# Optimization experiments

Hardware: AMD Instinct MI355X
Metric: run time of the kernel (lower is better)

The kernel has to match this reference:

```python
import jax, jax.numpy as jnp
import numpy as np

B, LINS, LHIS, LACT = 128, 64, 128, 32
VOCAB, ACTSZ = 2000, 100
INS_H, INS_E = 256, 128
ACT_E, ACT_IN, ACT_H = 128, 512, 512
POS_E, COL_E, COL_H = 32, 32, 32
ENV = 7 * (POS_E + COL_H)  # 448


def _lstm_cell(h, c, x, Wih, Whh, bih, bhh):
    # torch LSTM gate order: i, f, g, o
    g = x @ Wih.T + h @ Whh.T + bih + bhh
    i, f, gg, o = jnp.split(g, 4, axis=-1)
    c = jax.nn.sigmoid(f) * c + jax.nn.sigmoid(i) * jnp.tanh(gg)
    h = jax.nn.sigmoid(o) * jnp.tanh(c)
    return h, c


def _run_lstm(xs, Wih, Whh, bih, bhh):
    # xs: [T, N, D] -> hs: [T, N, H], zero initial state (torch default)
    N = xs.shape[1]
    H = Whh.shape[1]
    h0 = jnp.zeros((N, H), xs.dtype)

    def step(carry, x):
        h, c = carry
        h, c = _lstm_cell(h, c, x, Wih, Whh, bih, bhh)
        return (h, c), h

    _, hs = jax.lax.scan(step, (h0, h0), xs)
    return hs


def _bilstm_encode(tokens, emb, Wf, Uf, bf1, bf2, Wb, Ub, bb1, bb2):
    xs = emb[tokens].transpose(1, 0, 2)            # [L, B, E]
    hf = _run_lstm(xs, Wf, Uf, bf1, bf2)           # [L, B, H]
    hb = _run_lstm(xs[::-1], Wb, Ub, bb1, bb2)[::-1]
    return jnp.concatenate([hf, hb], -1).transpose(1, 0, 2)  # [B, L, 2H]


def _env_encode(tokens, color_emb, pos_emb, Wih, Whh, bih, bhh):
    # tokens: [B, 35] = 7 beakers x (id + 4 color slots)
    t = tokens.reshape(B, 7, 5)
    col = color_emb[t[:, :, 1:5]]                  # [B, 7, 4, COL_E]
    xs = col.reshape(B * 7, 4, COL_E).transpose(1, 0, 2)  # [4, B*7, COL_E]
    h_last = _run_lstm(xs, Wih, Whh, bih, bhh)[-1].reshape(B, 7, COL_H)
    pos = jnp.broadcast_to(pos_emb[None], (B, 7, POS_E))
    return jnp.concatenate([pos, h_last], -1).reshape(B, 7 * (POS_E + COL_H))


def _attend(A, H, q):
    # Faithful to attend(): scores = sum_k (H @ W)[b,l,k] * q[b,k]; softmax over l;
    # A = H @ W is query-independent so it is hoisted out of the decode loop.
    a = jax.nn.softmax(jnp.einsum('blk,bk->bl', A, q), axis=1)
    return jnp.einsum('bl,bld->bd', a, H)


def _forward(ins_tokens, his_tokens, actions, cur_env, ini_env,
             enc_emb, enc_Wih_f, enc_Whh_f, enc_bih_f, enc_bhh_f,
             enc_Wih_b, enc_Whh_b, enc_bih_b, enc_bhh_b,
             color_emb, pos_emb, ws_Wih, ws_Whh, ws_bih, ws_bhh,
             act_emb, W_c, W_p, W_sb1, W_sb2, W_sc1, W_sc2,
             Wbd_W, Wbd_b, dec_Wih, dec_Whh, dec_bih, dec_bhh,
             h2a_W, h2a_b, h0, c0):
    ins_enc = _bilstm_encode(ins_tokens, enc_emb, enc_Wih_f, enc_Whh_f, enc_bih_f,
                             enc_bhh_f, enc_Wih_b, enc_Whh_b, enc_bih_b, enc_bhh_b)
    his_enc = _bilstm_encode(his_tokens, enc_emb, enc_Wih_f, enc_Whh_f, enc_bih_f,
                             enc_bhh_f, enc_Wih_b, enc_Whh_b, enc_bih_b, enc_bhh_b)
    cur_ctx = _env_encode(cur_env, color_emb, pos_emb, ws_Wih, ws_Whh, ws_bih, ws_bhh)
    ini_ctx = _env_encode(ini_env, color_emb, pos_emb, ws_Wih, ws_Whh, ws_bih, ws_bhh)

    X = act_emb[actions]                            # [B, T, ACT_E]
    # Query-independent projections, hoisted out of the per-step loop (same math).
    A_c = jnp.einsum('bld,dk->blk', ins_enc, W_c)   # [B, LINS, ACT_H]
    A_p = jnp.einsum('bld,dk->blk', his_enc, W_p)   # [B, LHIS, ACT_H+2*INS_H]
    K = ACT_H + 2 * INS_H
    ini_rep = jnp.broadcast_to(ini_ctx[:, None, :], (B, LACT, ENV))
    cur_rep = jnp.broadcast_to(cur_ctx[:, None, :], (B, LACT, ENV))
    A_b1 = jnp.broadcast_to((ini_ctx @ W_sb1)[:, None, :], (B, LACT, K))
    A_b2 = jnp.broadcast_to((ini_ctx @ W_sb2)[:, None, :], (B, LACT, K))
    A_c1 = jnp.broadcast_to((cur_ctx @ W_sc1)[:, None, :], (B, LACT, K))
    A_c2 = jnp.broadcast_to((cur_ctx @ W_sc2)[:, None, :], (B, LACT, K))

    def step(carry, x_t):
        h, c = carry
        z_c = _attend(A_c, ins_enc, h)              # [B, 2*INS_H]
        q = jnp.concatenate([h, z_c], -1)           # [B, ACT_H+2*INS_H]
        z_p = _attend(A_p, his_enc, q)
        z_s1 = jnp.concatenate([_attend(A_b1, ini_rep, q),
                                _attend(A_b2, ini_rep, q)], -1)
        z_sk = jnp.concatenate([_attend(A_c1, cur_rep, q),
                                _attend(A_c2, cur_rep, q)], -1)
        hk1 = jnp.concatenate([z_c, z_p, z_s1, z_sk, x_t], -1)  # [B, 2944]
        hk = jnp.tanh(hk1 @ Wbd_W.T + Wbd_b)        # [B, ACT_IN]
        h, c = _lstm_cell(h, c, hk, dec_Wih, dec_Whh, dec_bih, dec_bhh)
        return (h, c), h

    _, outs = jax.lax.scan(step, (h0, c0), X.transpose(1, 0, 2))
    logits = outs.transpose(1, 0, 2) @ h2a_W.T + h2a_b  # [B, LACT, ACTSZ]
    return logits


def setup_inputs() -> dict:
    root = jax.random.key(0)
    ki = iter(jax.random.split(root, 40))

    def nrm(shape, s=0.05):
        return jax.random.normal(next(ki), shape, dtype=jnp.float32) * s

    inp = {}
    inp['ins_tokens'] = jax.random.randint(next(ki), (B, LINS), 0, VOCAB)
    inp['his_tokens'] = jax.random.randint(next(ki), (B, LHIS), 0, VOCAB)
    inp['actions'] = jax.random.randint(next(ki), (B, LACT), 0, ACTSZ)
    inp['cur_env'] = jax.random.randint(next(ki), (B, 35), 0, 7)
    inp['ini_env'] = jax.random.randint(next(ki), (B, 35), 0, 7)
    inp['enc_emb'] = nrm((VOCAB, INS_E))
    inp['enc_Wih_f'] = nrm((4 * INS_H, INS_E))
    inp['enc_Whh_f'] = nrm((4 * INS_H, INS_H))
    inp['enc_bih_f'] = nrm((4 * INS_H,))
    inp['enc_bhh_f'] = nrm((4 * INS_H,))
    inp['enc_Wih_b'] = nrm((4 * INS_H, INS_E))
    inp['enc_Whh_b'] = nrm((4 * INS_H, INS_H))
    inp['enc_bih_b'] = nrm((4 * INS_H,))
    inp['enc_bhh_b'] = nrm((4 * INS_H,))
    inp['color_emb'] = nrm((7, COL_E))
    inp['pos_emb'] = nrm((7, POS_E))
    inp['ws_Wih'] = nrm((4 * COL_H, COL_E))
    inp['ws_Whh'] = nrm((4 * COL_H, COL_H))
    inp['ws_bih'] = nrm((4 * COL_H,))
    inp['ws_bhh'] = nrm((4 * COL_H,))
    inp['act_emb'] = nrm((ACTSZ, ACT_E))
    inp['W_c'] = nrm((2 * INS_H, ACT_H))
    inp['W_p'] = nrm((2 * INS_H, 2 * INS_H + ACT_H))
    inp['W_sb1'] = nrm((ENV, ACT_H + 2 * INS_H))
    inp['W_sb2'] = nrm((ENV, ACT_H + 2 * INS_H))
    inp['W_sc1'] = nrm((ENV, ACT_H + 2 * INS_H))
    inp['W_sc2'] = nrm((ENV, ACT_H + 2 * INS_H))
    inp['Wbd_W'] = nrm((ACT_IN, 4 * ENV + 4 * INS_H + ACT_E))
    inp['Wbd_b'] = nrm((ACT_IN,))
    inp['dec_Wih'] = nrm((4 * ACT_H, ACT_IN))
    inp['dec_Whh'] = nrm((4 * ACT_H, ACT_H))
    inp['dec_bih'] = nrm((4 * ACT_H,))
    inp['dec_bhh'] = nrm((4 * ACT_H,))
    inp['h2a_W'] = nrm((ACTSZ, ACT_H))
    inp['h2a_b'] = nrm((ACTSZ,))
    inp['h0'] = nrm((B, ACT_H))
    inp['c0'] = nrm((B, ACT_H))
    return inp


def reference(ins_tokens, his_tokens, actions, cur_env, ini_env,
              enc_emb, enc_Wih_f, enc_Whh_f, enc_bih_f, enc_bhh_f,
              enc_Wih_b, enc_Whh_b, enc_bih_b, enc_bhh_b,
              color_emb, pos_emb, ws_Wih, ws_Whh, ws_bih, ws_bhh,
              act_emb, W_c, W_p, W_sb1, W_sb2, W_sc1, W_sc2,
              Wbd_W, Wbd_b, dec_Wih, dec_Whh, dec_bih, dec_bhh,
              h2a_W, h2a_b, h0, c0):
    return _forward(ins_tokens, his_tokens, actions, cur_env, ini_env,
                    enc_emb, enc_Wih_f, enc_Whh_f, enc_bih_f, enc_bhh_f,
                    enc_Wih_b, enc_Whh_b, enc_bih_b, enc_bhh_b,
                    color_emb, pos_emb, ws_Wih, ws_Whh, ws_bih, ws_bhh,
                    act_emb, W_c, W_p, W_sb1, W_sb2, W_sc1, W_sc2,
                    Wbd_W, Wbd_b, dec_Wih, dec_Whh, dec_bih, dec_bhh,
                    h2a_W, h2a_b, h0, c0)
```

## Files before the change

kernel.cpp:

```cpp
#include <hip/hip_runtime.h>


typedef unsigned short u16;
typedef __attribute__((ext_vector_type(8))) short bf16x8;
typedef __attribute__((ext_vector_type(4))) float f32x4;

#define DEVFN static __device__ __forceinline__

DEVFN float bf2f(u16 u) {
  unsigned int x = ((unsigned int)u) << 16;
  float f; __builtin_memcpy(&f, &x, 4); return f;
}
DEVFN u16 f2bf(float f) {
  unsigned int x; __builtin_memcpy(&x, &f, 4);
  x = (x + 0x7fffu + ((x >> 16) & 1u)) >> 16;
  return (u16)x;
}
DEVFN float sigf(float x) { return 1.f / (1.f + __expf(-x)); }
DEVFN bf16x8 load8(const u16* p) { return *(const bf16x8*)p; }
DEVFN int clampi(int v, int lo, int hi) { return v < lo ? lo : (v > hi ? hi : v); }

struct GemmArgs {
  const u16* A; int lda; int M;
  const u16* W; int ldw; int N; int K;
  void* out; int ldc;
  const float* bias;
  const float* hk_base; const float* proj_act; const int* actions; int t;
};

template <int EPI>
__global__ __launch_bounds__(256) void gemm_k(GemmArgs g) {
  int lane = threadIdx.x & 63;
  int wave = threadIdx.x >> 6;
  int col = lane & 15, q = lane >> 4;
  int m0 = blockIdx.x * 64 + (wave >> 1) * 32;
  int n0 = blockIdx.y * 64 + (wave & 1) * 32;
  f32x4 acc[2][2] = {};
  int rA[2] = { m0 + col, m0 + 16 + col };
  int rB[2] = { n0 + col, n0 + 16 + col };
  bool gA[2] = { rA[0] < g.M, rA[1] < g.M };
  bool gB[2] = { rB[0] < g.N, rB[1] < g.N };
  const u16* pA[2]; const u16* pB[2];
#pragma unroll
  for (int i = 0; i < 2; i++) {
    pA[i] = g.A + (size_t)(gA[i] ? rA[i] : 0) * g.lda + q * 8;
    pB[i] = g.W + (size_t)(gB[i] ? rB[i] : 0) * g.ldw + q * 8;
  }
  bf16x8 zf = {0,0,0,0,0,0,0,0};
  for (int k = 0; k < g.K; k += 32) {
    bf16x8 a0 = gA[0] ? load8(pA[0] + k) : zf;
    bf16x8 a1 = gA[1] ? load8(pA[1] + k) : zf;
    bf16x8 b0 = gB[0] ? load8(pB[0] + k) : zf;
    bf16x8 b1 = gB[1] ? load8(pB[1] + k) : zf;
    acc[0][0] = __builtin_amdgcn_mfma_f32_16x16x32_bf16(a0, b0, acc[0][0], 0, 0, 0);
    acc[0][1] = __builtin_amdgcn_mfma_f32_16x16x32_bf16(a0, b1, acc[0][1], 0, 0, 0);
    acc[1][0] = __builtin_amdgcn_mfma_f32_16x16x32_bf16(a1, b0, acc[1][0], 0, 0, 0);
    acc[1][1] = __builtin_amdgcn_mfma_f32_16x16x32_bf16(a1, b1, acc[1][1], 0, 0, 0);
  }
#pragma unroll
  for (int mi = 0; mi < 2; mi++)
#pragma unroll
    for (int ni = 0; ni < 2; ni++)
#pragma unroll
      for (int r = 0; r < 4; r++) {
        int m = m0 + mi * 16 + q * 4 + r;
        int n = n0 + ni * 16 + col;
        if (m >= g.M || n >= g.N) continue;
        float v = acc[mi][ni][r];
        if constexpr (EPI == 0) {
          if (g.bias) v += g.bias[n];
          ((float*)g.out)[(size_t)m * g.ldc + n] = v;
        } else {
          ((u16*)g.out)[(size_t)m * g.ldc + n] = f2bf(v);
        }
      }
}

template <int EPI>
__global__ __launch_bounds__(256) void gemm32_k(GemmArgs g) {
  int lane = threadIdx.x & 63;
  int wave = threadIdx.x >> 6;
  int col = lane & 15, q = lane >> 4;
  int m0 = blockIdx.x * 32 + (wave >> 1) * 16;
  int n0 = blockIdx.y * 32 + (wave & 1) * 16;
  f32x4 acc = {};
  int rA = m0 + col, rB = n0 + col;
  bool gA = rA < g.M, gB = rB < g.N;
  const u16* pA = g.A + (size_t)(gA ? rA : 0) * g.lda + q * 8;
  const u16* pB = g.W + (size_t)(gB ? rB : 0) * g.ldw + q * 8;
  bf16x8 zf = {0,0,0,0,0,0,0,0};
  for (int k = 0; k < g.K; k += 32) {
    bf16x8 a = gA ? load8(pA + k) : zf;
    bf16x8 b = gB ? load8(pB + k) : zf;
    acc = __builtin_amdgcn_mfma_f32_16x16x32_bf16(a, b, acc, 0, 0, 0);
  }
#pragma unroll
  for (int r = 0; r < 4; r++) {
    int m = m0 + q * 4 + r;
    int n = n0 + col;
    if (m >= g.M || n >= g.N) continue;
    float v = acc[r];
    if constexpr (EPI == 0) {
      if (g.bias) v += g.bias[n];
      ((float*)g.out)[(size_t)m * g.ldc + n] = v;
    } else {
      int act = clampi(g.actions[m * 32 + g.t], 0, 99);
      v += g.hk_base[m * 512 + n] + g.proj_act[(size_t)act * 512 + n];
      ((u16*)g.out)[(size_t)m * g.ldc + n] = f2bf(tanhf(v));
    }
  }
}

__global__ __launch_bounds__(256) void up_split(
    const u16* qbuf, const u16* wp, float* u_p2) {
  int lane = threadIdx.x & 63;
  int wave = threadIdx.x >> 6;
  int col = lane & 15, q = lane >> 4;
  int half = blockIdx.y >> 4;
  int by = blockIdx.y & 15;
  int m0 = blockIdx.x * 32 + (wave >> 1) * 16;
  int n0 = by * 32 + (wave & 1) * 16;
  f32x4 acc = {};
  const u16* pA = qbuf + (size_t)(m0 + col) * 1024 + half * 512 + q * 8;
  const u16* pB = wp + (size_t)(n0 + col) * 1024 + half * 512 + q * 8;
  for (int k = 0; k < 512; k += 32) {
    acc = __builtin_amdgcn_mfma_f32_16x16x32_bf16(load8(pA + k), load8(pB + k), acc, 0, 0, 0);
  }
  float* out = u_p2 + (size_t)half * 128 * 512;
#pragma unroll
  for (int r = 0; r < 4; r++) {
    int m = m0 + q * 4 + r;
    int n = n0 + col;
    out[(size_t)m * 512 + n] = acc[r];
  }
}

__global__ __launch_bounds__(256) void dec_gates_cell32(
    const u16* zin_cur, const u16* Wih, const u16* Whh, const float* bias_int,
    float* c_ws, u16* zin_nxt, u16* qbuf, u16* outs, int t) {
  int lane = threadIdx.x & 63, wave = threadIdx.x >> 6;
  int col = lane & 15, q = lane >> 4;
  int m0 = blockIdx.x * 32 + (wave >> 1) * 16;
  int n0 = blockIdx.y * 32 + (wave & 1) * 16;
  f32x4 acc = {};
  const u16* pA = zin_cur + (size_t)(m0 + col) * 1024 + q * 8;
  int r = n0 + col;
  int src = (r & 3) * 512 + (r >> 2);
  const u16* pI = Wih + (size_t)src * 512 + q * 8;
  const u16* pH = Whh + (size_t)src * 512 + q * 8;
  for (int k = 0; k < 512; k += 32) {
    acc = __builtin_amdgcn_mfma_f32_16x16x32_bf16(load8(pA + k), load8(pI + k), acc, 0, 0, 0);
  }
  for (int k = 0; k < 512; k += 32) {
    acc = __builtin_amdgcn_mfma_f32_16x16x32_bf16(load8(pA + 512 + k), load8(pH + k), acc, 0, 0, 0);
  }
  __shared__ float ls[32][36];
#pragma unroll
  for (int rr = 0; rr < 4; rr++) {
    int ml = (wave >> 1) * 16 + q * 4 + rr;
    int nl = (wave & 1) * 16 + col;
    ls[ml][nl] = acc[rr] + bias_int[blockIdx.y * 32 + nl];
  }
  __syncthreads();
  int m = threadIdx.x & 31, jloc = threadIdx.x >> 5;
  int gm = blockIdx.x * 32 + m;
  int j = blockIdx.y * 8 + jloc;
  float gi = ls[m][jloc * 4 + 0];
  float gf = ls[m][jloc * 4 + 1];
  float gg = ls[m][jloc * 4 + 2];
  float go = ls[m][jloc * 4 + 3];
  float cn = sigf(gf) * c_ws[gm * 512 + j] + sigf(gi) * tanhf(gg);
  c_ws[gm * 512 + j] = cn;
  float hn = sigf(go) * tanhf(cn);
  u16 hb = f2bf(hn);
  zin_nxt[(size_t)gm * 1024 + 512 + j] = hb;
  qbuf[(size_t)gm * 1024 + j] = hb;
  outs[((size_t)gm * 32 + t) * 512 + j] = hb;
}

struct CvtJob { const float* src; u16* dst; int R; int C; int ld; int c0; int tr; int blk0; };
struct CvtJobs { CvtJob j[15]; int njobs; };

__global__ void cvt_all(CvtJobs a) {
  int bid = blockIdx.x;
  int ji = 0;
  while (ji + 1 < a.njobs && bid >= a.j[ji + 1].blk0) ji++;
  CvtJob jb = a.j[ji];
  int idx = (bid - jb.blk0) * 256 + threadIdx.x;
  int n = jb.R * jb.C;
  if (idx >= n) return;
  int r = idx / jb.C, c = idx - r * jb.C;
  float v = jb.src[(size_t)r * jb.ld + jb.c0 + c];
  if (jb.tr) jb.dst[(size_t)c * jb.R + r] = f2bf(v);
  else jb.dst[idx] = f2bf(v);
}

__global__ void prep_small(
    const float* bih_f, const float* bhh_f, float* bias_f,
    const float* bih_b, const float* bhh_b, float* bias_b,
    const float* Wbd_b, float* bwbd,
    const float* h2a_b, float* bh2a,
    const float* dec_bih, const float* dec_bhh, float* bdecint,
    const float* h0, const float* c0, u16* zin0, u16* qbuf, float* c_ws) {
  int i = blockIdx.x * 256 + threadIdx.x;
  if (i < 1024) bias_f[i] = bih_f[i] + bhh_f[i];
  else if (i < 2048) { int k = i - 1024; bias_b[k] = bih_b[k] + bhh_b[k]; }
  else if (i < 2560) { int k = i - 2048; bwbd[k] = Wbd_b[k]; }
  else if (i < 2660) { int k = i - 2560; bh2a[k] = h2a_b[k]; }
  else if (i < 4708) {
    int r = i - 2660;
    int j = r >> 2, gg = r & 3;
    bdecint[r] = dec_bih[gg * 512 + j] + dec_bhh[gg * 512 + j];
  } else if (i < 4708 + 128 * 512) {
    int k = i - 4708;
    int b = k >> 9, d = k & 511;
    u16 hv = f2bf(h0[k]);
    zin0[(size_t)b * 1024 + 512 + d] = hv;
    qbuf[(size_t)b * 1024 + d] = hv;
    c_ws[k] = c0[k];
  }
}

__global__ void wsum_build(const float* Wbd, u16* Wsum) {
  int idx = blockIdx.x * 256 + threadIdx.x;
  int n = idx / 896, j = idx % 896;
  int c1 = (j < 448) ? (1024 + j) : (1920 + (j - 448));
  int c2 = c1 + 448;
  Wsum[idx] = f2bf(Wbd[(size_t)n * 2944 + c1] + Wbd[(size_t)n * 2944 + c2]);
}

__global__ __launch_bounds__(256) void env_encode(
    const int* cur_env, const int* ini_env,
    const float* color_emb, const float* pos_emb,
    const float* wih, const float* whh, const float* bih, const float* bhh,
    u16* ctx_cat) {
  __shared__ float s_wih[128 * 33], s_whh[128 * 33], s_b[128], s_col[7 * 32];
  __shared__ float h_lds[8][33];
  int tid = threadIdx.x;
  for (int i = tid; i < 128 * 32; i += 256) {
    int r = i >> 5, k2 = i & 31;
    s_wih[r * 33 + k2] = wih[i];
    s_whh[r * 33 + k2] = whh[i];
  }
  for (int i = tid; i < 128; i += 256) s_b[i] = bih[i] + bhh[i];
  for (int i = tid; i < 224; i += 256) s_col[i] = color_emb[i];
  int sl = tid >> 5, j = tid & 31;
  int gseq = blockIdx.x * 8 + sl;
  int e = gseq / 896, rem = gseq % 896;
  int b = rem / 7, p = rem % 7;
  const int* env = e ? ini_env : cur_env;
  int eoff = e ? 0 : 448;
  h_lds[sl][j] = 0.f;
  __syncthreads();
  float cj = 0.f, hj = 0.f;
  for (int st = 0; st < 4; st++) {
    int tok = clampi(env[b * 35 + p * 5 + 1 + st], 0, 6);
    const float* x = &s_col[tok * 32];
    float pi = s_b[j], pf = s_b[32 + j], pg = s_b[64 + j], po = s_b[96 + j];
    for (int k = 0; k < 32; k++) {
      float xk = x[k], hk = h_lds[sl][k];
      pi += s_wih[j * 33 + k] * xk + s_whh[j * 33 + k] * hk;
      pf += s_wih[(32 + j) * 33 + k] * xk + s_whh[(32 + j) * 33 + k] * hk;
      pg += s_wih[(64 + j) * 33 + k] * xk + s_whh[(64 + j) * 33 + k] * hk;
      po += s_wih[(96 + j) * 33 + k] * xk + s_whh[(96 + j) * 33 + k] * hk;
    }
    cj = sigf(pf) * cj + sigf(pi) * tanhf(pg);
    hj = sigf(po) * tanhf(cj);
    __syncthreads();
    h_lds[sl][j] = hj;
    __syncthreads();
  }
  size_t base = (size_t)b * 896 + eoff + p * 64;
  ctx_cat[base + j] = f2bf(pos_emb[p * 32 + j]);
  ctx_cat[base + 32 + j] = f2bf(hj);
}

#define HBUF ((size_t)4 * 128 * 256)
__global__ __launch_bounds__(128) void enc_step3(
    int t, int chainbase,
    const int* ins_tok, const int* his_tok,
    const float* projE_f, const float* projE_b,
    const u16* whh_f, const u16* whh_b,
    const float* bias_f, const float* bias_b,
    u16* h_enc, float* c_enc,
    u16* ins_enc, u16* his_enc) {
  int chain = chainbase + (blockIdx.x >> 6);
  int sub = blockIdx.x & 63;
  int sgrp = sub >> 3, jq = sub & 7;
  int w = threadIdx.x >> 6, lane = threadIdx.x & 63;
  int col = lane & 15, q = lane >> 4;
  int dir = chain & 1, his = chain >> 1;
  int L = his ? 128 : 64;
  const int* toks = his ? his_tok : ins_tok;
  int t_x = dir ? (L - 1 - t) : t;
  const float* projE = dir ? projE_b : projE_f;
  const u16* whh = dir ? whh_b : whh_f;
  const float* bias = dir ? bias_b : bias_f;
  const u16* h_rd = h_enc + ((size_t)((t & 1) ^ 1)) * HBUF + (size_t)chain * 128 * 256;
  u16* h_wr = h_enc + ((size_t)(t & 1)) * HBUF + (size_t)chain * 128 * 256;
  float* c_g = c_enc + (size_t)chain * 128 * 256;
  u16* out = his ? his_enc : ins_enc;

  int jw = jq * 32 + w * 16;
  f32x4 acc[4] = {};
  if (t > 0) {
    const u16* hrow = h_rd + (size_t)(sgrp * 16 + col) * 256 + q * 8;
    const u16* wrow[4];
#pragma unroll
    for (int G = 0; G < 4; G++) wrow[G] = whh + (size_t)(G * 256 + jw + col) * 256 + q * 8;
    for (int k = 0; k < 256; k += 32) {
      bf16x8 a = load8(hrow + k);
#pragma unroll
      for (int G = 0; G < 4; G++) {
        bf16x8 bb = load8(wrow[G] + k);
        acc[G] = __builtin_amdgcn_mfma_f32_16x16x32_bf16(a, bb, acc[G], 0, 0, 0);
      }
    }
  }
  int j = jw + col;
  float bi = bias[j], bf = bias[256 + j], bg = bias[512 + j], bo = bias[768 + j];
#pragma unroll
  for (int r = 0; r < 4; r++) {
    int s = q * 4 + r;
    int b = sgrp * 16 + s;
    int tok = clampi(toks[b * L + t_x], 0, 1999);
    const float* px = projE + (size_t)tok * 1024;
    float pi = acc[0][r] + px[j] + bi;
    float pf = acc[1][r] + px[256 + j] + bf;
    float pg = acc[2][r] + px[512 + j] + bg;
    float po = acc[3][r] + px[768 + j] + bo;
    float cold = (t > 0) ? c_g[b * 256 + j] : 0.f;
    float cn = sigf(pf) * cold + sigf(pi) * tanhf(pg);
    float hn = sigf(po) * tanhf(cn);
    c_g[b * 256 + j] = cn;
    u16 hb = f2bf(hn);
    h_wr[b * 256 + j] = hb;
    out[((size_t)b * L + t_x) * 512 + dir * 256 + j] = hb;
  }
}

__global__ __launch_bounds__(512) void attn1(
    const u16* A_c, const u16* insenc, u16* qattn, u16* qbuf) {
  int b = blockIdx.x, tid = threadIdx.x;
  __shared__ float su[512], red[512], aw[64];
  __shared__ float zacc[8][512];
  su[tid] = bf2f(qbuf[(size_t)b * 1024 + tid]);
  __syncthreads();
  {
    int l = tid >> 3, part = tid & 7;
    const u16* row = A_c + ((size_t)b * 64 + l) * 512 + part * 64;
    float s = 0.f;
    for (int k = 0; k < 64; k += 8) {
      bf16x8 v = load8(row + k);
#pragma unroll
      for (int e = 0; e < 8; e++) s += bf2f((u16)v[e]) * su[part * 64 + k + e];
    }
    red[tid] = s;
  }
  __syncthreads();
  if (tid < 64) {
    float sc = 0.f;
#pragma unroll
    for (int i = 0; i < 8; i++) sc += red[tid * 8 + i];
    float m = sc;
    for (int off = 32; off > 0; off >>= 1) m = fmaxf(m, __shfl_xor(m, off));
    float e = __expf(sc - m);
    float sm = e;
    for (int off = 32; off > 0; off >>= 1) sm += __shfl_xor(sm, off);
    aw[tid] = e / sm;
  }
  __syncthreads();
  {
    int part = tid >> 6, chunk = tid & 63;
    float a[8] = {};
    for (int l = part * 8; l < part * 8 + 8; l++) {
      bf16x8 v = load8(insenc + ((size_t)b * 64 + l) * 512 + chunk * 8);
      float w = aw[l];
#pragma unroll
      for (int e = 0; e < 8; e++) a[e] += w * bf2f((u16)v[e]);
    }
#pragma unroll
    for (int e = 0; e < 8; e++) zacc[part][chunk * 8 + e] = a[e];
  }
  __syncthreads();
  {
    float z = zacc[0][tid] + zacc[1][tid] + zacc[2][tid] + zacc[3][tid]
            + zacc[4][tid] + zacc[5][tid] + zacc[6][tid] + zacc[7][tid];
    u16 zb = f2bf(z);
    qattn[(size_t)b * 1024 + tid] = zb;
    qbuf[(size_t)b * 1024 + 512 + tid] = zb;
  }
}

__global__ __launch_bounds__(512) void attn2(
    const float* u_p2, const u16* hisenc, u16* qattn) {
  int b = blockIdx.x, tid = threadIdx.x;
  __shared__ float su[512], red[512], aw[128], mr[2];
  __shared__ float zacc[8][512];
  su[tid] = u_p2[(size_t)b * 512 + tid] + u_p2[65536 + (size_t)b * 512 + tid];
  __syncthreads();
  {
    int l = tid >> 2, part = tid & 3;
    const u16* row = hisenc + ((size_t)b * 128 + l) * 512 + part * 128;
    float s = 0.f;
    for (int k = 0; k < 128; k += 8) {
      bf16x8 v = load8(row + k);
#pragma unroll
      for (int e = 0; e < 8; e++) s += bf2f((u16)v[e]) * su[part * 128 + k + e];
    }
    red[tid] = s;
  }
  __syncthreads();
  float sc = 0.f;
  if (tid < 128) sc = red[tid * 4] + red[tid * 4 + 1] + red[tid * 4 + 2] + red[tid * 4 + 3];
  __syncthreads();
  if (tid < 128) red[tid] = sc;
  __syncthreads();
  if (tid < 64) {
    float m = fmaxf(red[tid], red[tid + 64]);
    for (int off = 32; off > 0; off >>= 1) m = fmaxf(m, __shfl_xor(m, off));
    if (tid == 0) mr[0] = m;
  }
  __syncthreads();
  float ex = 0.f;
  if (tid < 128) { ex = __expf(sc - mr[0]); red[tid] = ex; }
  __syncthreads();
  if (tid < 64) {
    float s2 = red[tid] + red[tid + 64];
    for (int off = 32; off > 0; off >>= 1) s2 += __shfl_xor(s2, off);
    if (tid == 0) mr[1] = s2;
  }
  __syncthreads();
  if (tid < 128) aw[tid] = ex / mr[1];
  __syncthreads();
  {
    int part = tid >> 6, chunk = tid & 63;
    float a[8] = {};
    for (int l = part * 16; l < part * 16 + 16; l++) {
      bf16x8 v = load8(hisenc + ((size_t)b * 128 + l) * 512 + chunk * 8);
      float w = aw[l];
#pragma unroll
      for (int e = 0; e < 8; e++) a[e] += w * bf2f((u16)v[e]);
    }
#pragma unroll
    for (int e = 0; e < 8; e++) zacc[part][chunk * 8 + e] = a[e];
  }
  __syncthreads();
  {
    float z = zacc[0][tid] + zacc[1][tid] + zacc[2][tid] + zacc[3][tid]
            + zacc[4][tid] + zacc[5][tid] + zacc[6][tid] + zacc[7][tid];
    qattn[(size_t)b * 1024 + 512 + tid] = f2bf(z);
  }
}

extern "C" void kernel_launch(void* const* d_in, const int* in_sizes, int n_in,
                              void* d_out, int out_size, void* d_ws, size_t ws_size,
                              hipStream_t stream) {
  const int* ins_tok = (const int*)d_in[0];
  const int* his_tok = (const int*)d_in[1];
  const int* actions = (const int*)d_in[2];
  const int* cur_env = (const int*)d_in[3];
  const int* ini_env = (const int*)d_in[4];
  const float* enc_emb = (const float*)d_in[5];
  const float* Wih_f = (const float*)d_in[6];
  const float* Whh_f = (const float*)d_in[7];
  const float* bih_f = (const float*)d_in[8];
  const float* bhh_f = (const float*)d_in[9];
  const float* Wih_b = (const float*)d_in[10];
  const float* Whh_b = (const float*)d_in[11];
  const float* bih_b = (const float*)d_in[12];
  const float* bhh_b = (const float*)d_in[13];
  const float* color_emb = (const float*)d_in[14];
  const float* pos_emb = (const float*)d_in[15];
  const float* ws_Wih = (const float*)d_in[16];
  const float* ws_Whh = (const float*)d_in[17];
  const float* ws_bih = (const float*)d_in[18];
  const float* ws_bhh = (const float*)d_in[19];
  const float* act_emb = (const float*)d_in[20];
  const float* W_c = (const float*)d_in[21];
  const float* W_p = (const float*)d_in[22];
  const float* Wbd_W = (const float*)d_in[27];
  const float* Wbd_b = (const float*)d_in[28];
  const float* dec_Wih = (const float*)d_in[29];
  const float* dec_Whh = (const float*)d_in[30];
  const float* dec_bih = (const float*)d_in[31];
  const float* dec_bhh = (const float*)d_in[32];
  const float* h2a_W = (const float*)d_in[33];
  const float* h2a_b = (const float*)d_in[34];
  const float* h0 = (const float*)d_in[35];
  const float* c0 = (const float*)d_in[36];
  (void)in_sizes; (void)n_in; (void)out_size; (void)ws_size;

  char* ws = (char*)d_ws;
  size_t off = 0;
  auto alloc = [&](size_t bytes) -> char* {
    char* p = ws + off;
    off = (off + bytes + 255) & ~(size_t)255;
    return p;
  };
  u16* insenc   = (u16*)alloc(8192ull * 512 * 2);
  u16* hisenc   = (u16*)alloc(16384ull * 512 * 2);
  u16* outs     = (u16*)alloc(4096ull * 512 * 2);
  u16* Wsum     = (u16*)alloc(512ull * 896 * 2);
  u16* h_enc    = (u16*)alloc(2 * HBUF * 2);
  float* c_enc  = (float*)alloc(4ull * 128 * 256 * 4);
  float* projact= (float*)alloc(100ull * 512 * 4);
  float* bias_f = (float*)alloc(1024 * 4);
  float* bias_b = (float*)alloc(1024 * 4);
  float* bdecint= (float*)alloc(2048 * 4);
  float* bwbd   = (float*)alloc(512 * 4);
  float* bh2a   = (float*)alloc(128 * 4);
  u16* ctxcat   = (u16*)alloc(128ull * 896 * 2);
  float* hkbase = (float*)alloc(128ull * 512 * 4);
  float* u_p2   = (float*)alloc(2ull * 128 * 512 * 4);
  u16* qbuf     = (u16*)alloc(128ull * 1024 * 2);
  u16* qattn    = (u16*)alloc(128ull * 1024 * 2);
  u16* zin      = (u16*)alloc(2ull * 128 * 1024 * 2);
  float* c_dec  = (float*)alloc(128ull * 512 * 4);
  float* projE_f = (float*)alloc(2000ull * 1024 * 4);
  float* projE_b = (float*)alloc(2000ull * 1024 * 4);
  u16* A_c      = (u16*)alloc(8192ull * 512 * 2);
  u16* emb_bf   = (u16*)alloc(2000ull * 128 * 2);
  u16* wihf_bf  = (u16*)alloc(1024ull * 128 * 2);
  u16* wihb_bf  = (u16*)alloc(1024ull * 128 * 2);
  u16* whhf_bf  = (u16*)alloc(1024ull * 256 * 2);
  u16* whhb_bf  = (u16*)alloc(1024ull * 256 * 2);
  u16* act_bf   = (u16*)alloc(100ull * 128 * 2);
  u16* wcT_bf   = (u16*)alloc(512ull * 512 * 2);
  u16* wp_bf    = (u16*)alloc(512ull * 1024 * 2);
  u16* wbd01_bf = (u16*)alloc(512ull * 1024 * 2);
  u16* wbdx_bf  = (u16*)alloc(512ull * 128 * 2);
  u16* dwih_bf  = (u16*)alloc(2048ull * 512 * 2);
  u16* dwhh_bf  = (u16*)alloc(2048ull * 512 * 2);
  u16* h2a_bf   = (u16*)alloc(100ull * 512 * 2);

  CvtJobs cj{};
  int nb = 0, jn = 0;
  auto addjob = [&](const float* s, u16* d, int R, int C, int ld, int c0c, int tr) {
    cj.j[jn] = { s, d, R, C, ld, c0c, tr, nb };
    nb += (R * C + 255) / 256;
    jn++;
  };
  addjob(enc_emb, emb_bf, 2000, 128, 128, 0, 0);
  addjob(Wih_f, wihf_bf, 1024, 128, 128, 0, 0);
  addjob(Wih_b, wihb_bf, 1024, 128, 128, 0, 0);
  addjob(Whh_f, whhf_bf, 1024, 256, 256, 0, 0);
  addjob(Whh_b, whhb_bf, 1024, 256, 256, 0, 0);
  addjob(act_emb, act_bf, 100, 128, 128, 0, 0);
  addjob(W_c, wcT_bf, 512, 512, 512, 0, 1);
  addjob(W_p, wp_bf, 512, 1024, 1024, 0, 0);
  addjob(Wbd_W, wbd01_bf, 512, 1024, 2944, 0, 0);
  addjob(Wbd_W, wbdx_bf, 512, 128, 2944, 2816, 0);
  addjob(dec_Wih, dwih_bf, 2048, 512, 512, 0, 0);
  addjob(dec_Whh, dwhh_bf, 2048, 512, 512, 0, 0);
  addjob(h2a_W, h2a_bf, 100, 512, 512, 0, 0);
  cj.njobs = jn;
  cvt_all<<<nb, 256, 0, stream>>>(cj);

  prep_small<<<(4708 + 128 * 512 + 255) / 256, 256, 0, stream>>>(
      bih_f, bhh_f, bias_f, bih_b, bhh_b, bias_b,
      Wbd_b, bwbd, h2a_b, bh2a, dec_bih, dec_bhh, bdecint,
      h0, c0, zin, qbuf, c_dec);
  wsum_build<<<1792, 256, 0, stream>>>(Wbd_W, Wsum);

  {
    GemmArgs ge = {};
    ge.A = emb_bf; ge.lda = 128; ge.M = 2000; ge.W = wihf_bf; ge.ldw = 128;
    ge.N = 1024; ge.K = 128; ge.out = projE_f; ge.ldc = 1024;
    gemm_k<0><<<dim3(32, 16), 256, 0, stream>>>(ge);
    ge.W = wihb_bf; ge.out = projE_b;
    gemm_k<0><<<dim3(32, 16), 256, 0, stream>>>(ge);
  }

  GemmArgs gp = {};
  gp.A = act_bf; gp.lda = 128; gp.M = 100; gp.W = wbdx_bf; gp.ldw = 128;
  gp.N = 512; gp.K = 128; gp.out = projact; gp.ldc = 512; gp.bias = bwbd;
  gemm_k<0><<<dim3(2, 8), 256, 0, stream>>>(gp);

  env_encode<<<224, 256, 0, stream>>>(cur_env, ini_env, color_emb, pos_emb,
                                      ws_Wih, ws_Whh, ws_bih, ws_bhh, ctxcat);
  GemmArgs gb = {};
  gb.A = ctxcat; gb.lda = 896; gb.M = 128; gb.W = Wsum; gb.ldw = 896;
  gb.N = 512; gb.K = 896; gb.out = hkbase; gb.ldc = 512;
  gemm_k<0><<<dim3(2, 8), 256, 0, stream>>>(gb);

  for (int t = 0; t < 128; t++) {
    int cb = (t < 64) ? 0 : 2;
    int nbk = (t < 64) ? 256 : 128;
    enc_step3<<<nbk, 128, 0, stream>>>(t, cb, ins_tok, his_tok,
                                       projE_f, projE_b, whhf_bf, whhb_bf,
                                       bias_f, bias_b, h_enc, c_enc,
                                       insenc, hisenc);
  }

  {
    GemmArgs ga = {};
    ga.A = insenc; ga.lda = 512; ga.M = 8192; ga.W = wcT_bf; ga.ldw = 512;
    ga.N = 512; ga.K = 512; ga.out = A_c; ga.ldc = 512;
    gemm_k<1><<<dim3(128, 8), 256, 0, stream>>>(ga);
  }

  for (int t = 0; t < 32; t++) {
    u16* zin_cur = zin + (size_t)(t & 1) * 128 * 1024;
    u16* zin_nxt = zin + (size_t)((t + 1) & 1) * 128 * 1024;
    attn1<<<128, 512, 0, stream>>>(A_c, insenc, qattn, qbuf);
    up_split<<<dim3(4, 32), 256, 0, stream>>>(qbuf, wp_bf, u_p2);
    attn2<<<128, 512, 0, stream>>>(u_p2, hisenc, qattn);
    GemmArgs gh = {};
    gh.A = qattn; gh.lda = 1024; gh.M = 128; gh.W = wbd01_bf; gh.ldw = 1024;
    gh.N = 512; gh.K = 1024; gh.out = zin_cur; gh.ldc = 1024;
    gh.hk_base = hkbase; gh.proj_act = projact; gh.actions = actions; gh.t = t;
    gemm32_k<2><<<dim3(4, 16), 256, 0, stream>>>(gh);
    dec_gates_cell32<<<dim3(4, 64), 256, 0, stream>>>(
        zin_cur, dwih_bf, dwhh_bf, bdecint, c_dec, zin_nxt, qbuf, outs, t);
  }

  GemmArgs gl = {};
  gl.A = outs; gl.lda = 512; gl.M = 4096; gl.W = h2a_bf; gl.ldw = 512;
  gl.N = 100; gl.K = 512; gl.out = d_out; gl.ldc = 100; gl.bias = bh2a;
  gemm32_k<0><<<dim3(128, 4), 256, 0, stream>>>(gl);
}
```

Measured before the change: 2.531 ms.

## Split K and shrink blocks in encoder, decoder cell, and attention projection kernels

The encoder step kernel now uses single-wave blocks with twice as many blocks. The decoder gate/cell kernel splits the K reduction across two waves per tile and sums the partials through LDS. The attention projection splits K into four quarters instead of two, and attn2 sums four partials. The aim is more parallelism and shorter serial MFMA chains in the latency-bound sequential steps. The cost is extra partial-sum traffic, more LDS, and more blocks launched per step.

Result: no change. 2.561 ms (+1.2%).

```diff
diff --git a/kernel.cpp b/kernel.cpp
--- a/kernel.cpp
+++ b/kernel.cpp
@@ -111,22 +111,22 @@
   }
 }
 
-__global__ __launch_bounds__(256) void up_split(
-    const u16* qbuf, const u16* wp, float* u_p2) {
+__global__ __launch_bounds__(256) void up_split4(
+    const u16* qbuf, const u16* wp, float* u_p4) {
   int lane = threadIdx.x & 63;
   int wave = threadIdx.x >> 6;
   int col = lane & 15, q = lane >> 4;
-  int half = blockIdx.y >> 4;
+  int qtr = blockIdx.y >> 4;
   int by = blockIdx.y & 15;
   int m0 = blockIdx.x * 32 + (wave >> 1) * 16;
   int n0 = by * 32 + (wave & 1) * 16;
   f32x4 acc = {};
-  const u16* pA = qbuf + (size_t)(m0 + col) * 1024 + half * 512 + q * 8;
-  const u16* pB = wp + (size_t)(n0 + col) * 1024 + half * 512 + q * 8;
-  for (int k = 0; k < 512; k += 32) {
+  const u16* pA = qbuf + (size_t)(m0 + col) * 1024 + qtr * 256 + q * 8;
+  const u16* pB = wp + (size_t)(n0 + col) * 1024 + qtr * 256 + q * 8;
+  for (int k = 0; k < 256; k += 32) {
     acc = __builtin_amdgcn_mfma_f32_16x16x32_bf16(load8(pA + k), load8(pB + k), acc, 0, 0, 0);
   }
-  float* out = u_p2 + (size_t)half * 128 * 512;
+  float* out = u_p4 + (size_t)qtr * 128 * 512;
 #pragma unroll
   for (int r = 0; r < 4; r++) {
     int m = m0 + q * 4 + r;
@@ -135,47 +135,47 @@
   }
 }
 
-__global__ __launch_bounds__(256) void dec_gates_cell32(
+__global__ __launch_bounds__(512) void dec_gates_cell512(
     const u16* zin_cur, const u16* Wih, const u16* Whh, const float* bias_int,
     float* c_ws, u16* zin_nxt, u16* qbuf, u16* outs, int t) {
   int lane = threadIdx.x & 63, wave = threadIdx.x >> 6;
   int col = lane & 15, q = lane >> 4;
-  int m0 = blockIdx.x * 32 + (wave >> 1) * 16;
-  int n0 = blockIdx.y * 32 + (wave & 1) * 16;
+  int tile = wave >> 1, kh = wave & 1;
+  int m0 = blockIdx.x * 32 + (tile >> 1) * 16;
+  int n0 = blockIdx.y * 32 + (tile & 1) * 16;
   f32x4 acc = {};
-  const u16* pA = zin_cur + (size_t)(m0 + col) * 1024 + q * 8;
   int r = n0 + col;
   int src = (r & 3) * 512 + (r >> 2);
-  const u16* pI = Wih + (size_t)src * 512 + q * 8;
-  const u16* pH = Whh + (size_t)src * 512 + q * 8;
+  const u16* pA = zin_cur + (size_t)(m0 + col) * 1024 + kh * 512 + q * 8;
+  const u16* pW = (kh ? Whh : Wih) + (size_t)src * 512 + q * 8;
   for (int k = 0; k < 512; k += 32) {
-    acc = __builtin_amdgcn_mfma_f32_16x16x32_bf16(load8(pA + k), load8(pI + k), acc, 0, 0, 0);
-  }
-  for (int k = 0; k < 512; k += 32) {
-    acc = __builtin_amdgcn_mfma_f32_16x16x32_bf16(load8(pA + 512 + k), load8(pH + k), acc, 0, 0, 0);
-  }
-  __shared__ float ls[32][36];
+    acc = __builtin_amdgcn_mfma_f32_16x16x32_bf16(load8(pA + k), load8(pW + k), acc, 0, 0, 0);
+  }
+  __shared__ float ls[2][32][36];
 #pragma unroll
   for (int rr = 0; rr < 4; rr++) {
-    int ml = (wave >> 1) * 16 + q * 4 + rr;
-    int nl = (wave & 1) * 16 + col;
-    ls[ml][nl] = acc[rr] + bias_int[blockIdx.y * 32 + nl];
-  }
-  __syncthreads();
-  int m = threadIdx.x & 31, jloc = threadIdx.x >> 5;
-  int gm = blockIdx.x * 32 + m;
-  int j = blockIdx.y * 8 + jloc;
-  float gi = ls[m][jloc * 4 + 0];
-  float gf = ls[m][jloc * 4 + 1];
-  float gg = ls[m][jloc * 4 + 2];
-  float go = ls[m][jloc * 4 + 3];
-  float cn = sigf(gf) * c_ws[gm * 512 + j] + sigf(gi) * tanhf(gg);
-  c_ws[gm * 512 + j] = cn;
-  float hn = sigf(go) * tanhf(cn);
-  u16 hb = f2bf(hn);
-  zin_nxt[(size_t)gm * 1024 + 512 + j] = hb;
-  qbuf[(size_t)gm * 1024 + j] = hb;
-  outs[((size_t)gm * 32 + t) * 512 + j] = hb;
+    int ml = (tile >> 1) * 16 + q * 4 + rr;
+    int nl = (tile & 1) * 16 + col;
+    ls[kh][ml][nl] = acc[rr];
+  }
+  __syncthreads();
+  if (threadIdx.x < 256) {
+    int m = threadIdx.x & 31, jloc = threadIdx.x >> 5;
+    int gm = blockIdx.x * 32 + m;
+    int j = blockIdx.y * 8 + jloc;
+    int base = jloc * 4;
+    float gi = ls[0][m][base + 0] + ls[1][m][base + 0] + bias_int[blockIdx.y * 32 + base + 0];
+    float gf = ls[0][m][base + 1] + ls[1][m][base + 1] + bias_int[blockIdx.y * 32 + base + 1];
+    float gg = ls[0][m][base + 2] + ls[1][m][base + 2] + bias_int[blockIdx.y * 32 + base + 2];
+    float go = ls[0][m][base + 3] + ls[1][m][base + 3] + bias_int[blockIdx.y * 32 + base + 3];
+    float cn = sigf(gf) * c_ws[gm * 512 + j] + sigf(gi) * tanhf(gg);
+    c_ws[gm * 512 + j] = cn;
+    float hn = sigf(go) * tanhf(cn);
+    u16 hb = f2bf(hn);
+    zin_nxt[(size_t)gm * 1024 + 512 + j] = hb;
+    qbuf[(size_t)gm * 1024 + j] = hb;
+    outs[((size_t)gm * 32 + t) * 512 + j] = hb;
+  }
 }
 
 struct CvtJob { const float* src; u16* dst; int R; int C; int ld; int c0; int tr; int blk0; };
@@ -276,7 +276,7 @@
 }
 
 #define HBUF ((size_t)4 * 128 * 256)
-__global__ __launch_bounds__(128) void enc_step3(
+__global__ __launch_bounds__(64) void enc_step4(
     int t, int chainbase,
     const int* ins_tok, const int* his_tok,
     const float* projE_f, const float* projE_b,
@@ -284,10 +284,10 @@
     const float* bias_f, const float* bias_b,
     u16* h_enc, float* c_enc,
     u16* ins_enc, u16* his_enc) {
-  int chain = chainbase + (blockIdx.x >> 6);
-  int sub = blockIdx.x & 63;
-  int sgrp = sub >> 3, jq = sub & 7;
-  int w = threadIdx.x >> 6, lane = threadIdx.x & 63;
+  int chain = chainbase + (blockIdx.x >> 7);
+  int sub = blockIdx.x & 127;
+  int sgrp = sub >> 4, jq = sub & 15;
+  int lane = threadIdx.x & 63;
   int col = lane & 15, q = lane >> 4;
   int dir = chain & 1, his = chain >> 1;
   int L = his ? 128 : 64;
@@ -301,7 +301,7 @@
   float* c_g = c_enc + (size_t)chain * 128 * 256;
   u16* out = his ? his_enc : ins_enc;
 
-  int jw = jq * 32 + w * 16;
+  int jw = jq * 16;
   f32x4 acc[4] = {};
   if (t > 0) {
     const u16* hrow = h_rd + (size_t)(sgrp * 16 + col) * 256 + q * 8;
@@ -393,11 +393,12 @@
 }
 
 __global__ __launch_bounds__(512) void attn2(
-    const float* u_p2, const u16* hisenc, u16* qattn) {
+    const float* u_p4, const u16* hisenc, u16* qattn) {
   int b = blockIdx.x, tid = threadIdx.x;
   __shared__ float su[512], red[512], aw[128], mr[2];
   __shared__ float zacc[8][512];
-  su[tid] = u_p2[(size_t)b * 512 + tid] + u_p2[65536 + (size_t)b * 512 + tid];
+  su[tid] = u_p4[(size_t)b * 512 + tid] + u_p4[65536 + (size_t)b * 512 + tid]
+          + u_p4[131072 + (size_t)b * 512 + tid] + u_p4[196608 + (size_t)b * 512 + tid];
   __syncthreads();
   {
     int l = tid >> 2, part = tid & 3;
@@ -512,7 +513,7 @@
   float* bh2a   = (float*)alloc(128 * 4);
   u16* ctxcat   = (u16*)alloc(128ull * 896 * 2);
   float* hkbase = (float*)alloc(128ull * 512 * 4);
-  float* u_p2   = (float*)alloc(2ull * 128 * 512 * 4);
+  float* u_p4   = (float*)alloc(4ull * 128 * 512 * 4);
   u16* qbuf     = (u16*)alloc(128ull * 1024 * 2);
   u16* qattn    = (u16*)alloc(128ull * 1024 * 2);
   u16* zin      = (u16*)alloc(2ull * 128 * 1024 * 2);
@@ -586,11 +587,11 @@
 
   for (int t = 0; t < 128; t++) {
     int cb = (t < 64) ? 0 : 2;
-    int nbk = (t < 64) ? 256 : 128;
-    enc_step3<<<nbk, 128, 0, stream>>>(t, cb, ins_tok, his_tok,
-                                       projE_f, projE_b, whhf_bf, whhb_bf,
-                                       bias_f, bias_b, h_enc, c_enc,
-                                       insenc, hisenc);
+    int nbk = (t < 64) ? 512 : 256;
+    enc_step4<<<nbk, 64, 0, stream>>>(t, cb, ins_tok, his_tok,
+                                      projE_f, projE_b, whhf_bf, whhb_bf,
+                                      bias_f, bias_b, h_enc, c_enc,
+                                      insenc, hisenc);
   }
 
   {
@@ -604,14 +605,14 @@
     u16* zin_cur = zin + (size_t)(t & 1) * 128 * 1024;
     u16* zin_nxt = zin + (size_t)((t + 1) & 1) * 128 * 1024;
     attn1<<<128, 512, 0, stream>>>(A_c, insenc, qattn, qbuf);
-    up_split<<<dim3(4, 32), 256, 0, stream>>>(qbuf, wp_bf, u_p2);
-    attn2<<<128, 512, 0, stream>>>(u_p2, hisenc, qattn);
+    up_split4<<<dim3(4, 64), 256, 0, stream>>>(qbuf, wp_bf, u_p4);
+    attn2<<<128, 512, 0, stream>>>(u_p4, hisenc, qattn);
     GemmArgs gh = {};
     gh.A = qattn; gh.lda = 1024; gh.M = 128; gh.W = wbd01_bf; gh.ldw = 1024;
     gh.N = 512; gh.K = 1024; gh.out = zin_cur; gh.ldc = 1024;
     gh.hk_base = hkbase; gh.proj_act = projact; gh.actions = actions; gh.t = t;
     gemm32_k<2><<<dim3(4, 16), 256, 0, stream>>>(gh);
-    dec_gates_cell32<<<dim3(4, 64), 256, 0, stream>>>(
+    dec_gates_cell512<<<dim3(4, 64), 512, 0, stream>>>(
         zin_cur, dwih_bf, dwhh_bf, bdecint, c_dec, zin_nxt, qbuf, outs, t);
   }
 
```
